# Kernel tuning notes

Measured on AMD Instinct MI355X. Metric: run time of the kernel, lower is better.

The kernel has to match this reference:

```python
import jax, jax.numpy as jnp
import numpy as np

T, D = 4096, 1024  # seq_len, hidden dim (input dim must equal hidden dim due to residual)


def setup_inputs() -> dict:
    key = jax.random.key(0)
    ks = jax.random.split(key, 12)
    s = 1.0 / np.sqrt(D).astype(np.float32)  # lecun-normal-ish scale
    w = lambda k: jax.random.normal(k, (D, D), jnp.float32) * s
    return {
        "xs": jax.random.normal(ks[0], (T, D), jnp.float32),
        # flax param 'initial_state' uses nn.initializers.normal() (stddev=1e-2)
        "init_state": jax.random.normal(ks[1], (D,), jnp.float32) * 0.01,
        # GRUCell input->hidden dense (with bias) for r, z, n gates
        "Wir": w(ks[2]), "Wiz": w(ks[3]), "Win": w(ks[4]),
        "bir": jnp.zeros((D,), jnp.float32),
        "biz": jnp.zeros((D,), jnp.float32),
        "bin_": jnp.zeros((D,), jnp.float32),
        # GRUCell hidden->hidden dense: r,z have no bias; n-gate hidden dense has bias
        "Whr": w(ks[5]), "Whz": w(ks[6]), "Whn": w(ks[7]),
        "bhn": jnp.zeros((D,), jnp.float32),
        # post dense + layernorm
        "Wl": w(ks[8]), "bl": jnp.zeros((D,), jnp.float32),
        "ln_scale": jnp.ones((D,), jnp.float32),
        "ln_bias": jnp.zeros((D,), jnp.float32),
    }


def reference(xs, init_state, Wir, Wiz, Win, bir, biz, bin_, Whr, Whz, Whn, bhn,
              Wl, bl, ln_scale, ln_bias):
    # flax.linen.GRUCell recurrence, scanned over time (axis 0)
    def step(h, x):
        r = jax.nn.sigmoid(x @ Wir + bir + h @ Whr)
        z = jax.nn.sigmoid(x @ Wiz + biz + h @ Whz)
        n = jnp.tanh(x @ Win + bin_ + r * (h @ Whn + bhn))
        h_new = (1.0 - z) * n + z * h
        return h_new, h_new

    _, ys = jax.lax.scan(step, init_state, xs)  # ys: [T, D]

    # relu -> dropout(rate=0, identity) -> dense -> residual -> layernorm
    lin = jax.nn.relu(ys) @ Wl + bl
    y = xs + lin
    mu = jnp.mean(y, axis=-1, keepdims=True)
    var = jnp.var(y, axis=-1, keepdims=True)
    return (y - mu) / jnp.sqrt(var + 1e-6) * ln_scale + ln_bias
```

## Files before the change

kernel.cpp:

```cpp
#include <hip/hip_runtime.h>
#include <math.h>

#define Dh 1024
#define Tt 4096
#define NB 128

template<bool RELU, bool RESID>
__global__ __launch_bounds__(256)
void gemm64(const float* __restrict__ A, const float* __restrict__ B,
            const float* __restrict__ bias, const float* __restrict__ resid,
            float* __restrict__ C, int M, int N, int K, int ldc)
{
    __shared__ __align__(16) float As[16][68];
    __shared__ __align__(16) float Bs[16][64];
    const int tid = threadIdx.x;
    const int tx = tid & 15, ty = tid >> 4;
    const int bn = blockIdx.x * 64, bm = blockIdx.y * 64;

    const int lm = tid >> 2, lk = (tid & 3) * 4;
    const int bk = tid >> 4, bn4 = (tid & 15) * 4;

    float acc[4][4] = {};

    for (int k0 = 0; k0 < K; k0 += 16) {
        float4 av = *(const float4*)(A + (size_t)(bm + lm) * K + k0 + lk);
        if (RELU) {
            av.x = fmaxf(av.x, 0.f); av.y = fmaxf(av.y, 0.f);
            av.z = fmaxf(av.z, 0.f); av.w = fmaxf(av.w, 0.f);
        }
        As[lk + 0][lm] = av.x; As[lk + 1][lm] = av.y;
        As[lk + 2][lm] = av.z; As[lk + 3][lm] = av.w;
        *(float4*)&Bs[bk][bn4] = *(const float4*)(B + (size_t)(k0 + bk) * N + bn + bn4);
        __syncthreads();
        #pragma unroll
        for (int kk = 0; kk < 16; ++kk) {
            float4 a4 = *(const float4*)&As[kk][ty * 4];
            float4 b4 = *(const float4*)&Bs[kk][tx * 4];
            acc[0][0] += a4.x * b4.x; acc[0][1] += a4.x * b4.y; acc[0][2] += a4.x * b4.z; acc[0][3] += a4.x * b4.w;
            acc[1][0] += a4.y * b4.x; acc[1][1] += a4.y * b4.y; acc[1][2] += a4.y * b4.z; acc[1][3] += a4.y * b4.w;
            acc[2][0] += a4.z * b4.x; acc[2][1] += a4.z * b4.y; acc[2][2] += a4.z * b4.z; acc[2][3] += a4.z * b4.w;
            acc[3][0] += a4.w * b4.x; acc[3][1] += a4.w * b4.y; acc[3][2] += a4.w * b4.z; acc[3][3] += a4.w * b4.w;
        }
        __syncthreads();
    }

    const float4 bias4 = *(const float4*)(bias + bn + tx * 4);
    #pragma unroll
    for (int i = 0; i < 4; ++i) {
        const int row = bm + ty * 4 + i;
        float4 o;
        o.x = acc[i][0] + bias4.x; o.y = acc[i][1] + bias4.y;
        o.z = acc[i][2] + bias4.z; o.w = acc[i][3] + bias4.w;
        if (RESID) {
            const float4 r4 = *(const float4*)(resid + (size_t)row * N + bn + tx * 4);
            o.x += r4.x; o.y += r4.y; o.z += r4.z; o.w += r4.w;
        }
        *(float4*)(C + (size_t)row * ldc + bn + tx * 4) = o;
    }
}

__device__ __forceinline__ float fast_sigmoid(float x)
{
    return __builtin_amdgcn_rcpf(1.f + __expf(-x));
}
__device__ __forceinline__ float fast_tanh(float x)
{
    x = fminf(15.f, fmaxf(-15.f, x));
    const float e2 = __expf(2.f * x);
    return (e2 - 1.f) * __builtin_amdgcn_rcpf(e2 + 1.f);
}

__global__ __launch_bounds__(256)
void pack_h0(const float* __restrict__ h0, unsigned long long* __restrict__ buf)
{
    const int idx = blockIdx.x * 256 + threadIdx.x;
    __hip_atomic_store(buf + idx, (unsigned long long)__float_as_uint(h0[idx]),
                       __ATOMIC_RELAXED, __HIP_MEMORY_SCOPE_AGENT);
}

__global__ __launch_bounds__(320, 1)
void gru_rec(const float* __restrict__ xproj,
             const float* __restrict__ Whr, const float* __restrict__ Whz,
             const float* __restrict__ Whn, const float* __restrict__ bhn,
             float* __restrict__ ys,
             unsigned long long* __restrict__ hbuf)
{
    const int b = blockIdx.x, tid = threadIdx.x;
    const bool is_compute = tid < 256;
    const int g = tid >> 5;
    const int i = tid & 31;
    const int col = b * 8 + g;

    __shared__ __align__(16) float h_lds[Dh];
    __shared__ float hnew_lds[8];
    __shared__ float xp_lds[24];

    float wr[32], wz[32], wn[32];
    float bhn_c = 0.f;
    if (is_compute) {
        #pragma unroll
        for (int j = 0; j < 8; ++j)
            #pragma unroll
            for (int k = 0; k < 4; ++k) {
                const int r = 4 * i + 128 * j + k;
                wr[j * 4 + k] = Whr[(size_t)r * Dh + col];
                wz[j * 4 + k] = Whz[(size_t)r * Dh + col];
                wn[j * 4 + k] = Whn[(size_t)r * Dh + col];
            }
        bhn_c = bhn[col];
    } else {
        const int lane = tid - 256;
        if (lane < 24)
            xp_lds[lane] = xproj[(size_t)(lane >> 3) * Dh + b * 8 + (lane & 7)];
    }
    __syncthreads();

    for (int t = 0; t < Tt; ++t) {
        const unsigned long long* src = hbuf + (size_t)(t & 1) * Dh;
        unsigned long long*       dst = hbuf + (size_t)((t + 1) & 1) * Dh;
        const unsigned int want = (unsigned int)t;

        float4 y0, y1, y2, y3;

        if (is_compute) {
            unsigned long long p0, p1, p2, p3;
            int tries = 0;
            for (;;) {
                p0 = __hip_atomic_load(src + tid +   0, __ATOMIC_RELAXED, __HIP_MEMORY_SCOPE_AGENT);
                p1 = __hip_atomic_load(src + tid + 256, __ATOMIC_RELAXED, __HIP_MEMORY_SCOPE_AGENT);
                p2 = __hip_atomic_load(src + tid + 512, __ATOMIC_RELAXED, __HIP_MEMORY_SCOPE_AGENT);
                p3 = __hip_atomic_load(src + tid + 768, __ATOMIC_RELAXED, __HIP_MEMORY_SCOPE_AGENT);
                unsigned int bad = ((unsigned int)(p0 >> 32)) ^ want;
                bad |= ((unsigned int)(p1 >> 32)) ^ want;
                bad |= ((unsigned int)(p2 >> 32)) ^ want;
                bad |= ((unsigned int)(p3 >> 32)) ^ want;
                if (!bad) break;
                if (++tries > 6) __builtin_amdgcn_s_sleep(1);
            }
            h_lds[tid +   0] = __uint_as_float((unsigned int)p0);
            h_lds[tid + 256] = __uint_as_float((unsigned int)p1);
            h_lds[tid + 512] = __uint_as_float((unsigned int)p2);
            h_lds[tid + 768] = __uint_as_float((unsigned int)p3);
        }
        __syncthreads();

        if (is_compute) {
            float ar = 0.f, az = 0.f, an = 0.f;
            const float4* h4 = (const float4*)h_lds;
            #pragma unroll
            for (int j = 0; j < 8; ++j) {
                const float4 hv = h4[i + j * 32];
                ar += hv.x * wr[4*j] + hv.y * wr[4*j+1] + hv.z * wr[4*j+2] + hv.w * wr[4*j+3];
                az += hv.x * wz[4*j] + hv.y * wz[4*j+1] + hv.z * wz[4*j+2] + hv.w * wz[4*j+3];
                an += hv.x * wn[4*j] + hv.y * wn[4*j+1] + hv.z * wn[4*j+2] + hv.w * wn[4*j+3];
            }
            #pragma unroll
            for (int off = 16; off > 0; off >>= 1) {
                ar += __shfl_down(ar, off, 32);
                az += __shfl_down(az, off, 32);
                an += __shfl_down(an, off, 32);
            }

            if (i == 0) {
                const float xr = xp_lds[g], xz = xp_lds[8 + g], xn = xp_lds[16 + g];
                const float r = fast_sigmoid(xr + ar);
                const float z = fast_sigmoid(xz + az);
                const float n = fast_tanh(xn + r * (an + bhn_c));
                const float hp = h_lds[col];
                hnew_lds[g] = (1.f - z) * n + z * hp;
            }
        } else {
            const int lane = tid - 256;
            const float4* hr = (const float4*)(h_lds + lane * 16);
            y0 = hr[0]; y1 = hr[1]; y2 = hr[2]; y3 = hr[3];
        }
        __syncthreads();

        if (!is_compute) {
            const int lane = tid - 256;
            if (lane < 8) {
                const unsigned long long packed =
                    ((unsigned long long)(unsigned int)(t + 1) << 32) |
                    (unsigned long long)__float_as_uint(hnew_lds[lane]);
                __hip_atomic_store(dst + b * 8 + lane, packed,
                                   __ATOMIC_RELAXED, __HIP_MEMORY_SCOPE_AGENT);
            }
            if (t > 0) {
                float4* yrow = (float4*)(ys + (size_t)(t - 1) * Dh) + lane * 4;
                yrow[0] = y0; yrow[1] = y1; yrow[2] = y2; yrow[3] = y3;
            }
            if (lane < 24 && t + 1 < Tt) {
                xp_lds[lane] = xproj[(size_t)(t + 1) * (3 * Dh)
                                     + (size_t)(lane >> 3) * Dh + b * 8 + (lane & 7)];
            }
        }
    }

    if (b == (Tt & (NB - 1)) && is_compute) {
        const unsigned long long* src = hbuf + (size_t)(Tt & 1) * Dh;
        const unsigned int want = (unsigned int)Tt;
        unsigned long long p0, p1, p2, p3;
        for (;;) {
            p0 = __hip_atomic_load(src + tid +   0, __ATOMIC_RELAXED, __HIP_MEMORY_SCOPE_AGENT);
            p1 = __hip_atomic_load(src + tid + 256, __ATOMIC_RELAXED, __HIP_MEMORY_SCOPE_AGENT);
            p2 = __hip_atomic_load(src + tid + 512, __ATOMIC_RELAXED, __HIP_MEMORY_SCOPE_AGENT);
            p3 = __hip_atomic_load(src + tid + 768, __ATOMIC_RELAXED, __HIP_MEMORY_SCOPE_AGENT);
            unsigned int bad = ((unsigned int)(p0 >> 32)) ^ want;
            bad |= ((unsigned int)(p1 >> 32)) ^ want;
            bad |= ((unsigned int)(p2 >> 32)) ^ want;
            bad |= ((unsigned int)(p3 >> 32)) ^ want;
            if (!bad) break;
        }
        float* yrow = ys + (size_t)(Tt - 1) * Dh;
        yrow[tid +   0] = __uint_as_float((unsigned int)p0);
        yrow[tid + 256] = __uint_as_float((unsigned int)p1);
        yrow[tid + 512] = __uint_as_float((unsigned int)p2);
        yrow[tid + 768] = __uint_as_float((unsigned int)p3);
    }
}

__global__ __launch_bounds__(256)
void layernorm_ip(float* __restrict__ y, const float* __restrict__ sc,
                  const float* __restrict__ bi)
{
    __shared__ float red[8], red2[8], stat[2];
    const int row = blockIdx.x, tid = threadIdx.x;
    float4* yr = (float4*)(y + (size_t)row * Dh);
    float4 v = yr[tid];
    float s  = v.x + v.y + v.z + v.w;
    float s2 = v.x*v.x + v.y*v.y + v.z*v.z + v.w*v.w;
    #pragma unroll
    for (int off = 32; off > 0; off >>= 1) {
        s  += __shfl_down(s,  off);
        s2 += __shfl_down(s2, off);
    }
    if ((tid & 63) == 0) { red[tid >> 6] = s; red2[tid >> 6] = s2; }
    __syncthreads();
    if (tid == 0) {
        float ts = 0.f, t2 = 0.f;
        #pragma unroll
        for (int w = 0; w < 4; ++w) { ts += red[w]; t2 += red2[w]; }
        const float mu  = ts / (float)Dh;
        const float var = t2 / (float)Dh - mu * mu;
        stat[0] = mu;
        stat[1] = rsqrtf(var + 1e-6f);
    }
    __syncthreads();
    const float mu = stat[0], rstd = stat[1];
    const float4 s4 = ((const float4*)sc)[tid];
    const float4 b4 = ((const float4*)bi)[tid];
    v.x = (v.x - mu) * rstd * s4.x + b4.x;
    v.y = (v.y - mu) * rstd * s4.y + b4.y;
    v.z = (v.z - mu) * rstd * s4.z + b4.z;
    v.w = (v.w - mu) * rstd * s4.w + b4.w;
    yr[tid] = v;
}

extern "C" void kernel_launch(void* const* d_in, const int* in_sizes, int n_in,
                              void* d_out, int out_size, void* d_ws, size_t ws_size,
                              hipStream_t stream)
{
    const float* xs   = (const float*)d_in[0];
    const float* h0   = (const float*)d_in[1];
    const float* Wir  = (const float*)d_in[2];
    const float* Wiz  = (const float*)d_in[3];
    const float* Win  = (const float*)d_in[4];
    const float* bir  = (const float*)d_in[5];
    const float* biz  = (const float*)d_in[6];
    const float* bin_ = (const float*)d_in[7];
    const float* Whr  = (const float*)d_in[8];
    const float* Whz  = (const float*)d_in[9];
    const float* Whn  = (const float*)d_in[10];
    const float* bhn  = (const float*)d_in[11];
    const float* Wl   = (const float*)d_in[12];
    const float* bl   = (const float*)d_in[13];
    const float* ln_s = (const float*)d_in[14];
    const float* ln_b = (const float*)d_in[15];
    float* out = (float*)d_out;

    float* xproj = (float*)d_ws;
    float* ys    = xproj + (size_t)Tt * 3 * Dh;
    unsigned long long* hbuf = (unsigned long long*)(ys + (size_t)Tt * Dh);

    pack_h0<<<4, 256, 0, stream>>>(h0, hbuf);

    dim3 ggrid(Dh / 64, Tt / 64);
    gemm64<false, false><<<ggrid, 256, 0, stream>>>(xs, Wir, bir, nullptr,
                                                    xproj + 0 * Dh, Tt, Dh, Dh, 3 * Dh);
    gemm64<false, false><<<ggrid, 256, 0, stream>>>(xs, Wiz, biz, nullptr,
                                                    xproj + 1 * Dh, Tt, Dh, Dh, 3 * Dh);
    gemm64<false, false><<<ggrid, 256, 0, stream>>>(xs, Win, bin_, nullptr,
                                                    xproj + 2 * Dh, Tt, Dh, Dh, 3 * Dh);

    gru_rec<<<NB, 320, 0, stream>>>(xproj, Whr, Whz, Whn, bhn, ys, hbuf);

    gemm64<true, true><<<ggrid, 256, 0, stream>>>(ys, Wl, bl, xs, out, Tt, Dh, Dh, Dh);
    layernorm_ip<<<Tt, 256, 0, stream>>>(out, ln_s, ln_b);
}
```

Measured before the change: 9.003 ms.

## Replicate hidden-state mailbox into 16 copies to spread polling contention

The single double-buffered hidden-state exchange buffer is replaced by 16 replicated copies. Each group of 8 blocks polls its own copy, and every block writes its 8 new values into all 16 copies. This is meant to cut contention from 128 blocks spinning on the same cache lines in the cross-block recurrence handshake, at the cost of 16x more global atomic stores per step. The ys row copy is also changed to a coalesced float4 stride pattern, and the final-row writer is moved to block 0.

```diff
diff --git a/kernel.cpp b/kernel.cpp
--- a/kernel.cpp
+++ b/kernel.cpp
@@ -4,6 +4,7 @@
 #define Dh 1024
 #define Tt 4096
 #define NB 128
+#define NCOPY 16
 
 template<bool RELU, bool RESID>
 __global__ __launch_bounds__(256)
@@ -74,7 +75,8 @@
 void pack_h0(const float* __restrict__ h0, unsigned long long* __restrict__ buf)
 {
     const int idx = blockIdx.x * 256 + threadIdx.x;
-    __hip_atomic_store(buf + idx, (unsigned long long)__float_as_uint(h0[idx]),
+    const int slot = idx & (Dh - 1);
+    __hip_atomic_store(buf + idx, (unsigned long long)__float_as_uint(h0[slot]),
                        __ATOMIC_RELAXED, __HIP_MEMORY_SCOPE_AGENT);
 }
 
@@ -83,7 +85,7 @@
              const float* __restrict__ Whr, const float* __restrict__ Whz,
              const float* __restrict__ Whn, const float* __restrict__ bhn,
              float* __restrict__ ys,
-             unsigned long long* __restrict__ hbuf)
+             unsigned long long* __restrict__ mbox)
 {
     const int b = blockIdx.x, tid = threadIdx.x;
     const bool is_compute = tid < 256;
@@ -115,9 +117,12 @@
     }
     __syncthreads();
 
+    const int mycopy = b >> 3;
+
     for (int t = 0; t < Tt; ++t) {
-        const unsigned long long* src = hbuf + (size_t)(t & 1) * Dh;
-        unsigned long long*       dst = hbuf + (size_t)((t + 1) & 1) * Dh;
+        const unsigned long long* src =
+            mbox + (size_t)(t & 1) * (NCOPY * Dh) + (size_t)mycopy * Dh;
+        unsigned long long* dstbase = mbox + (size_t)((t + 1) & 1) * (NCOPY * Dh);
         const unsigned int want = (unsigned int)t;
 
         float4 y0, y1, y2, y3;
@@ -171,23 +176,29 @@
             }
         } else {
             const int lane = tid - 256;
-            const float4* hr = (const float4*)(h_lds + lane * 16);
-            y0 = hr[0]; y1 = hr[1]; y2 = hr[2]; y3 = hr[3];
+            const float4* hr = (const float4*)h_lds;
+            y0 = hr[lane]; y1 = hr[lane + 64]; y2 = hr[lane + 128]; y3 = hr[lane + 192];
         }
         __syncthreads();
 
         if (!is_compute) {
             const int lane = tid - 256;
-            if (lane < 8) {
-                const unsigned long long packed =
-                    ((unsigned long long)(unsigned int)(t + 1) << 32) |
-                    (unsigned long long)__float_as_uint(hnew_lds[lane]);
-                __hip_atomic_store(dst + b * 8 + lane, packed,
-                                   __ATOMIC_RELAXED, __HIP_MEMORY_SCOPE_AGENT);
+            {
+                const int cp = lane >> 2, j2 = (lane & 3) * 2;
+                unsigned long long* dst = dstbase + (size_t)cp * Dh + b * 8 + j2;
+                const unsigned long long taghi =
+                    ((unsigned long long)(unsigned int)(t + 1) << 32);
+                const unsigned long long pk0 =
+                    taghi | (unsigned long long)__float_as_uint(hnew_lds[j2]);
+                const unsigned long long pk1 =
+                    taghi | (unsigned long long)__float_as_uint(hnew_lds[j2 + 1]);
+                __hip_atomic_store(dst + 0, pk0, __ATOMIC_RELAXED, __HIP_MEMORY_SCOPE_AGENT);
+                __hip_atomic_store(dst + 1, pk1, __ATOMIC_RELAXED, __HIP_MEMORY_SCOPE_AGENT);
             }
             if (t > 0) {
-                float4* yrow = (float4*)(ys + (size_t)(t - 1) * Dh) + lane * 4;
-                yrow[0] = y0; yrow[1] = y1; yrow[2] = y2; yrow[3] = y3;
+                float4* yrow = (float4*)(ys + (size_t)(t - 1) * Dh);
+                yrow[lane] = y0; yrow[lane + 64] = y1;
+                yrow[lane + 128] = y2; yrow[lane + 192] = y3;
             }
             if (lane < 24 && t + 1 < Tt) {
                 xp_lds[lane] = xproj[(size_t)(t + 1) * (3 * Dh)
@@ -196,8 +207,8 @@
         }
     }
 
-    if (b == (Tt & (NB - 1)) && is_compute) {
-        const unsigned long long* src = hbuf + (size_t)(Tt & 1) * Dh;
+    if (b == 0 && is_compute) {
+        const unsigned long long* src = mbox + (size_t)(Tt & 1) * (NCOPY * Dh);
         const unsigned int want = (unsigned int)Tt;
         unsigned long long p0, p1, p2, p3;
         for (;;) {
@@ -280,9 +291,9 @@
 
     float* xproj = (float*)d_ws;
     float* ys    = xproj + (size_t)Tt * 3 * Dh;
-    unsigned long long* hbuf = (unsigned long long*)(ys + (size_t)Tt * Dh);
-
-    pack_h0<<<4, 256, 0, stream>>>(h0, hbuf);
+    unsigned long long* mbox = (unsigned long long*)(ys + (size_t)Tt * Dh);
+
+    pack_h0<<<(NCOPY * Dh) / 256, 256, 0, stream>>>(h0, mbox);
 
     dim3 ggrid(Dh / 64, Tt / 64);
     gemm64<false, false><<<ggrid, 256, 0, stream>>>(xs, Wir, bir, nullptr,
@@ -292,7 +303,7 @@
     gemm64<false, false><<<ggrid, 256, 0, stream>>>(xs, Win, bin_, nullptr,
                                                     xproj + 2 * Dh, Tt, Dh, Dh, 3 * Dh);
 
-    gru_rec<<<NB, 320, 0, stream>>>(xproj, Whr, Whz, Whn, bhn, ys, hbuf);
+    gru_rec<<<NB, 320, 0, stream>>>(xproj, Whr, Whz, Whn, bhn, ys, mbox);
 
     gemm64<true, true><<<ggrid, 256, 0, stream>>>(ys, Wl, bl, xs, out, Tt, Dh, Dh, Dh);
     layernorm_ip<<<Tt, 256, 0, stream>>>(out, ln_s, ln_b);
```

Result: slower. 10.72 ms (+19.1%).

## Double-buffer LDS state and publish hidden values directly from compute lanes

Applied to the files above, without the earlier changes.

Double-buffers the hidden-state and input-projection LDS arrays by step parity. This removes the second __syncthreads per timestep. Compute lanes now publish their new hidden value straight to the global exchange buffer, so it no longer goes through a helper wave. The helper wave's row copy to ys is changed to coalesced float4 strides. The aim is to shorten the serial critical path of each recurrence step, at the cost of relying on parity buffering for correctness across steps.

```diff
diff --git a/kernel.cpp b/kernel.cpp
--- a/kernel.cpp
+++ b/kernel.cpp
@@ -91,9 +91,8 @@
     const int i = tid & 31;
     const int col = b * 8 + g;
 
-    __shared__ __align__(16) float h_lds[Dh];
-    __shared__ float hnew_lds[8];
-    __shared__ float xp_lds[24];
+    __shared__ __align__(16) float h_lds[2][Dh];
+    __shared__ float xp_lds[2][24];
 
     float wr[32], wz[32], wn[32];
     float bhn_c = 0.f;
@@ -111,16 +110,15 @@
     } else {
         const int lane = tid - 256;
         if (lane < 24)
-            xp_lds[lane] = xproj[(size_t)(lane >> 3) * Dh + b * 8 + (lane & 7)];
+            xp_lds[0][lane] = xproj[(size_t)(lane >> 3) * Dh + b * 8 + (lane & 7)];
     }
     __syncthreads();
 
     for (int t = 0; t < Tt; ++t) {
-        const unsigned long long* src = hbuf + (size_t)(t & 1) * Dh;
-        unsigned long long*       dst = hbuf + (size_t)((t + 1) & 1) * Dh;
+        const int par = t & 1;
+        const unsigned long long* src = hbuf + (size_t)par * Dh;
+        unsigned long long*       dst = hbuf + (size_t)(par ^ 1) * Dh;
         const unsigned int want = (unsigned int)t;
-
-        float4 y0, y1, y2, y3;
 
         if (is_compute) {
             unsigned long long p0, p1, p2, p3;
@@ -137,16 +135,16 @@
                 if (!bad) break;
                 if (++tries > 6) __builtin_amdgcn_s_sleep(1);
             }
-            h_lds[tid +   0] = __uint_as_float((unsigned int)p0);
-            h_lds[tid + 256] = __uint_as_float((unsigned int)p1);
-            h_lds[tid + 512] = __uint_as_float((unsigned int)p2);
-            h_lds[tid + 768] = __uint_as_float((unsigned int)p3);
+            h_lds[par][tid +   0] = __uint_as_float((unsigned int)p0);
+            h_lds[par][tid + 256] = __uint_as_float((unsigned int)p1);
+            h_lds[par][tid + 512] = __uint_as_float((unsigned int)p2);
+            h_lds[par][tid + 768] = __uint_as_float((unsigned int)p3);
         }
         __syncthreads();
 
         if (is_compute) {
             float ar = 0.f, az = 0.f, an = 0.f;
-            const float4* h4 = (const float4*)h_lds;
+            const float4* h4 = (const float4*)h_lds[par];
             #pragma unroll
             for (int j = 0; j < 8; ++j) {
                 const float4 hv = h4[i + j * 32];
@@ -162,41 +160,38 @@
             }
 
             if (i == 0) {
-                const float xr = xp_lds[g], xz = xp_lds[8 + g], xn = xp_lds[16 + g];
+                const float xr = xp_lds[par][g];
+                const float xz = xp_lds[par][8 + g];
+                const float xn = xp_lds[par][16 + g];
                 const float r = fast_sigmoid(xr + ar);
                 const float z = fast_sigmoid(xz + az);
                 const float n = fast_tanh(xn + r * (an + bhn_c));
-                const float hp = h_lds[col];
-                hnew_lds[g] = (1.f - z) * n + z * hp;
+                const float hp = h_lds[par][col];
+                const float hnew = (1.f - z) * n + z * hp;
+                const unsigned long long packed =
+                    ((unsigned long long)(unsigned int)(t + 1) << 32) |
+                    (unsigned long long)__float_as_uint(hnew);
+                __hip_atomic_store(dst + col, packed,
+                                   __ATOMIC_RELAXED, __HIP_MEMORY_SCOPE_AGENT);
             }
         } else {
             const int lane = tid - 256;
-            const float4* hr = (const float4*)(h_lds + lane * 16);
-            y0 = hr[0]; y1 = hr[1]; y2 = hr[2]; y3 = hr[3];
-        }
-        __syncthreads();
-
-        if (!is_compute) {
-            const int lane = tid - 256;
-            if (lane < 8) {
-                const unsigned long long packed =
-                    ((unsigned long long)(unsigned int)(t + 1) << 32) |
-                    (unsigned long long)__float_as_uint(hnew_lds[lane]);
-                __hip_atomic_store(dst + b * 8 + lane, packed,
-                                   __ATOMIC_RELAXED, __HIP_MEMORY_SCOPE_AGENT);
-            }
             if (t > 0) {
-                float4* yrow = (float4*)(ys + (size_t)(t - 1) * Dh) + lane * 4;
-                yrow[0] = y0; yrow[1] = y1; yrow[2] = y2; yrow[3] = y3;
+                const float4* hr = (const float4*)h_lds[par];
+                const float4 a = hr[lane], c = hr[lane + 64];
+                const float4 d = hr[lane + 128], e = hr[lane + 192];
+                float4* yrow = (float4*)(ys + (size_t)(t - 1) * Dh);
+                yrow[lane] = a; yrow[lane + 64] = c;
+                yrow[lane + 128] = d; yrow[lane + 192] = e;
             }
             if (lane < 24 && t + 1 < Tt) {
-                xp_lds[lane] = xproj[(size_t)(t + 1) * (3 * Dh)
-                                     + (size_t)(lane >> 3) * Dh + b * 8 + (lane & 7)];
-            }
-        }
-    }
-
-    if (b == (Tt & (NB - 1)) && is_compute) {
+                xp_lds[par ^ 1][lane] = xproj[(size_t)(t + 1) * (3 * Dh)
+                                              + (size_t)(lane >> 3) * Dh + b * 8 + (lane & 7)];
+            }
+        }
+    }
+
+    if (b == 0 && is_compute) {
         const unsigned long long* src = hbuf + (size_t)(Tt & 1) * Dh;
         const unsigned int want = (unsigned int)Tt;
         unsigned long long p0, p1, p2, p3;
```

After: 11.32 ms. 1.26x slower.

## Halve GRU recurrence blocks to 64 with 16 columns per block

Applied to the files above, without the earlier changes.

The persistent GRU recurrence kernel now runs 64 blocks of 576 threads instead of 128 blocks of 320, so each block computes 16 hidden columns with 16 compute warps plus one helper warp. Fewer blocks means fewer participants in the per-step cross-block flag exchange, and each thread polls only two packed h entries instead of four. In exchange each CU holds twice the register-resident weights and does more work per step, and the helper-warp code paths and final row writeback are re-indexed to match.

```diff
diff --git a/kernel.cpp b/kernel.cpp
--- a/kernel.cpp
+++ b/kernel.cpp
@@ -3,7 +3,7 @@
 
 #define Dh 1024
 #define Tt 4096
-#define NB 128
+#define NB 64
 
 template<bool RELU, bool RESID>
 __global__ __launch_bounds__(256)
@@ -78,7 +78,7 @@
                        __ATOMIC_RELAXED, __HIP_MEMORY_SCOPE_AGENT);
 }
 
-__global__ __launch_bounds__(320, 1)
+__global__ __launch_bounds__(576, 1)
 void gru_rec(const float* __restrict__ xproj,
              const float* __restrict__ Whr, const float* __restrict__ Whz,
              const float* __restrict__ Whn, const float* __restrict__ bhn,
@@ -86,14 +86,14 @@
              unsigned long long* __restrict__ hbuf)
 {
     const int b = blockIdx.x, tid = threadIdx.x;
-    const bool is_compute = tid < 256;
+    const bool is_compute = tid < 512;
     const int g = tid >> 5;
     const int i = tid & 31;
-    const int col = b * 8 + g;
+    const int col = b * 16 + g;
 
     __shared__ __align__(16) float h_lds[Dh];
-    __shared__ float hnew_lds[8];
-    __shared__ float xp_lds[24];
+    __shared__ float hnew_lds[16];
+    __shared__ float xp_lds[48];
 
     float wr[32], wz[32], wn[32];
     float bhn_c = 0.f;
@@ -109,9 +109,9 @@
             }
         bhn_c = bhn[col];
     } else {
-        const int lane = tid - 256;
-        if (lane < 24)
-            xp_lds[lane] = xproj[(size_t)(lane >> 3) * Dh + b * 8 + (lane & 7)];
+        const int lane = tid - 512;
+        if (lane < 48)
+            xp_lds[lane] = xproj[(size_t)(lane >> 4) * Dh + b * 16 + (lane & 15)];
     }
     __syncthreads();
 
@@ -123,24 +123,19 @@
         float4 y0, y1, y2, y3;
 
         if (is_compute) {
-            unsigned long long p0, p1, p2, p3;
+            const int s0 = tid * 2;
+            unsigned long long p0, p1;
             int tries = 0;
             for (;;) {
-                p0 = __hip_atomic_load(src + tid +   0, __ATOMIC_RELAXED, __HIP_MEMORY_SCOPE_AGENT);
-                p1 = __hip_atomic_load(src + tid + 256, __ATOMIC_RELAXED, __HIP_MEMORY_SCOPE_AGENT);
-                p2 = __hip_atomic_load(src + tid + 512, __ATOMIC_RELAXED, __HIP_MEMORY_SCOPE_AGENT);
-                p3 = __hip_atomic_load(src + tid + 768, __ATOMIC_RELAXED, __HIP_MEMORY_SCOPE_AGENT);
+                p0 = __hip_atomic_load(src + s0 + 0, __ATOMIC_RELAXED, __HIP_MEMORY_SCOPE_AGENT);
+                p1 = __hip_atomic_load(src + s0 + 1, __ATOMIC_RELAXED, __HIP_MEMORY_SCOPE_AGENT);
                 unsigned int bad = ((unsigned int)(p0 >> 32)) ^ want;
                 bad |= ((unsigned int)(p1 >> 32)) ^ want;
-                bad |= ((unsigned int)(p2 >> 32)) ^ want;
-                bad |= ((unsigned int)(p3 >> 32)) ^ want;
                 if (!bad) break;
                 if (++tries > 6) __builtin_amdgcn_s_sleep(1);
             }
-            h_lds[tid +   0] = __uint_as_float((unsigned int)p0);
-            h_lds[tid + 256] = __uint_as_float((unsigned int)p1);
-            h_lds[tid + 512] = __uint_as_float((unsigned int)p2);
-            h_lds[tid + 768] = __uint_as_float((unsigned int)p3);
+            h_lds[s0 + 0] = __uint_as_float((unsigned int)p0);
+            h_lds[s0 + 1] = __uint_as_float((unsigned int)p1);
         }
         __syncthreads();
 
@@ -162,7 +157,9 @@
             }
 
             if (i == 0) {
-                const float xr = xp_lds[g], xz = xp_lds[8 + g], xn = xp_lds[16 + g];
+                const float xr = xp_lds[g];
+                const float xz = xp_lds[16 + g];
+                const float xn = xp_lds[32 + g];
                 const float r = fast_sigmoid(xr + ar);
                 const float z = fast_sigmoid(xz + az);
                 const float n = fast_tanh(xn + r * (an + bhn_c));
@@ -170,52 +167,48 @@
                 hnew_lds[g] = (1.f - z) * n + z * hp;
             }
         } else {
-            const int lane = tid - 256;
-            const float4* hr = (const float4*)(h_lds + lane * 16);
-            y0 = hr[0]; y1 = hr[1]; y2 = hr[2]; y3 = hr[3];
+            const int lane = tid - 512;
+            const float4* hr = (const float4*)h_lds;
+            y0 = hr[lane]; y1 = hr[lane + 64]; y2 = hr[lane + 128]; y3 = hr[lane + 192];
         }
         __syncthreads();
 
         if (!is_compute) {
-            const int lane = tid - 256;
-            if (lane < 8) {
+            const int lane = tid - 512;
+            if (lane < 16) {
                 const unsigned long long packed =
                     ((unsigned long long)(unsigned int)(t + 1) << 32) |
                     (unsigned long long)__float_as_uint(hnew_lds[lane]);
-                __hip_atomic_store(dst + b * 8 + lane, packed,
+                __hip_atomic_store(dst + b * 16 + lane, packed,
                                    __ATOMIC_RELAXED, __HIP_MEMORY_SCOPE_AGENT);
             }
             if (t > 0) {
-                float4* yrow = (float4*)(ys + (size_t)(t - 1) * Dh) + lane * 4;
-                yrow[0] = y0; yrow[1] = y1; yrow[2] = y2; yrow[3] = y3;
-            }
-            if (lane < 24 && t + 1 < Tt) {
+                float4* yrow = (float4*)(ys + (size_t)(t - 1) * Dh);
+                yrow[lane] = y0; yrow[lane + 64] = y1;
+                yrow[lane + 128] = y2; yrow[lane + 192] = y3;
+            }
+            if (lane < 48 && t + 1 < Tt) {
                 xp_lds[lane] = xproj[(size_t)(t + 1) * (3 * Dh)
-                                     + (size_t)(lane >> 3) * Dh + b * 8 + (lane & 7)];
-            }
-        }
-    }
-
-    if (b == (Tt & (NB - 1)) && is_compute) {
+                                     + (size_t)(lane >> 4) * Dh + b * 16 + (lane & 15)];
+            }
+        }
+    }
+
+    if (b == 0 && is_compute) {
         const unsigned long long* src = hbuf + (size_t)(Tt & 1) * Dh;
         const unsigned int want = (unsigned int)Tt;
-        unsigned long long p0, p1, p2, p3;
+        const int s0 = tid * 2;
+        unsigned long long p0, p1;
         for (;;) {
-            p0 = __hip_atomic_load(src + tid +   0, __ATOMIC_RELAXED, __HIP_MEMORY_SCOPE_AGENT);
-            p1 = __hip_atomic_load(src + tid + 256, __ATOMIC_RELAXED, __HIP_MEMORY_SCOPE_AGENT);
-            p2 = __hip_atomic_load(src + tid + 512, __ATOMIC_RELAXED, __HIP_MEMORY_SCOPE_AGENT);
-            p3 = __hip_atomic_load(src + tid + 768, __ATOMIC_RELAXED, __HIP_MEMORY_SCOPE_AGENT);
+            p0 = __hip_atomic_load(src + s0 + 0, __ATOMIC_RELAXED, __HIP_MEMORY_SCOPE_AGENT);
+            p1 = __hip_atomic_load(src + s0 + 1, __ATOMIC_RELAXED, __HIP_MEMORY_SCOPE_AGENT);
             unsigned int bad = ((unsigned int)(p0 >> 32)) ^ want;
             bad |= ((unsigned int)(p1 >> 32)) ^ want;
-            bad |= ((unsigned int)(p2 >> 32)) ^ want;
-            bad |= ((unsigned int)(p3 >> 32)) ^ want;
             if (!bad) break;
         }
         float* yrow = ys + (size_t)(Tt - 1) * Dh;
-        yrow[tid +   0] = __uint_as_float((unsigned int)p0);
-        yrow[tid + 256] = __uint_as_float((unsigned int)p1);
-        yrow[tid + 512] = __uint_as_float((unsigned int)p2);
-        yrow[tid + 768] = __uint_as_float((unsigned int)p3);
+        yrow[s0 + 0] = __uint_as_float((unsigned int)p0);
+        yrow[s0 + 1] = __uint_as_float((unsigned int)p1);
     }
 }
 
@@ -292,7 +285,7 @@
     gemm64<false, false><<<ggrid, 256, 0, stream>>>(xs, Win, bin_, nullptr,
                                                     xproj + 2 * Dh, Tt, Dh, Dh, 3 * Dh);
 
-    gru_rec<<<NB, 320, 0, stream>>>(xproj, Whr, Whz, Whn, bhn, ys, hbuf);
+    gru_rec<<<NB, 576, 0, stream>>>(xproj, Whr, Whz, Whn, bhn, ys, hbuf);
 
     gemm64<true, true><<<ggrid, 256, 0, stream>>>(ys, Wl, bl, xs, out, Tt, Dh, Dh, Dh);
     layernorm_ip<<<Tt, 256, 0, stream>>>(out, ln_s, ln_b);
```

Result: faster. 8.258 ms (-8.3%).
